# Performance work log

Measured on AMD Instinct MI355X. Metric: run time of the kernel, lower is better.

The kernel has to match this reference:

```python
import jax, jax.numpy as jnp
import numpy as np

U, DP, TOPK, NH = 2, 16, 8, 2
D = 512
M = DP ** U          # 256 slots
DK = U * DP          # 32 addressing dim
BETA_MAX = 2.0


def setup_inputs():
    key = jax.random.key(0)
    ks = jax.random.split(key, 12)
    B, T = 8, 128
    s = 0.02
    return {
        "h": jax.random.normal(ks[0], (B, T, D), jnp.float32),
        "K_slots": jax.random.normal(ks[1], (B, M, D), jnp.float32) * s,
        "V_slots": jax.random.normal(ks[2], (B, M, D), jnp.float32) * s,
        "z_K": jnp.ones((B, M), jnp.float32),
        "z_V": jnp.ones((B, M), jnp.float32),
        "W_k": jax.random.normal(ks[3], (DK, D), jnp.float32) * s,
        "W_q": jax.random.normal(ks[4], (DK, D), jnp.float32) * s,
        "log_tau_w": jnp.zeros((1,), jnp.float32),
        "log_tau_r": jnp.zeros((1,), jnp.float32),
        "hh_k": jax.random.normal(ks[5], (NH, D, D), jnp.float32) * s,
        "hh_vk": jax.random.normal(ks[6], (NH, D, D), jnp.float32) * s,
        "hh_vv": jax.random.normal(ks[7], (NH, D, D), jnp.float32) * s,
        "hh_bw": jax.random.normal(ks[8], (NH, 1, D), jnp.float32) * s,
        "hh_bb": jnp.zeros((NH, 1), jnp.float32),
        "gamma": jnp.float32(1.0),
        "W_out": jax.random.normal(ks[9], (D, D), jnp.float32) * s,
        "W_gate": jax.random.normal(ks[10], (D, D), jnp.float32) * s,
    }


def _kron_address(z, log_tau):
    # z: [B, DK]; Kronecker-factored softmax address over M = DP**U slots
    B = z.shape[0]
    probs = jax.nn.softmax(z.reshape(B, U, DP) / jnp.exp(log_tau[0]), axis=-1)
    addr = probs[:, 0]
    for u in range(1, U):
        addr = (addr[:, :, None] * probs[:, u, None, :]).reshape(B, -1)
    w, idx = jax.lax.top_k(addr, TOPK)
    return idx, w


def _forward(h, K_slots, V_slots, z_K, z_V, W_k, W_q, log_tau_w, log_tau_r,
             hh_k, hh_vk, hh_vv, hh_bw, hh_bb, gamma, W_out, W_gate,
             checkpoint=False):
    B, T, _ = h.shape
    scale = D ** -0.5
    b_idx = jnp.arange(B)[:, None]
    sp_gamma = jax.nn.softplus(gamma)

    def step(carry, h_t):
        K_s, V_s, zK, zV = carry
        write_idx, write_w = _kron_address(h_t @ W_k.T, log_tau_w)
        read_idx, _ = _kron_address(h_t @ W_q.T, log_tau_r)
        # scatter write weights into dense [B, M] (top-k indices are unique)
        w_full = jnp.zeros((B, M), h_t.dtype).at[b_idx, write_idx].set(write_w)
        # PDMA decay
        decay = (1.0 - w_full) ** sp_gamma
        K_s = decay[..., None] * K_s
        V_s = decay[..., None] * V_s
        zK = decay * zK + w_full
        zV = decay * zV + w_full
        # gather active slots: [B, K, D]
        K_act = jnp.take_along_axis(K_s, write_idx[:, :, None], axis=1)
        V_act = jnp.take_along_axis(V_s, write_idx[:, :, None], axis=1)
        # Householder update chain
        for j in range(NH):
            k_j = jax.nn.silu(h_t @ hh_k[j].T)
            k_hat = k_j / jnp.maximum(
                jnp.linalg.norm(k_j, axis=-1, keepdims=True), 1e-12)
            v_kj = h_t @ hh_vk[j].T
            v_vj = h_t @ hh_vv[j].T
            beta = BETA_MAX * jax.nn.sigmoid(h_t @ hh_bw[j].T + hh_bb[j])  # [B,1]
            kh = k_hat[:, None, :]
            be = beta[:, None, :]
            K_act = K_act - be * kh * (kh * K_act).sum(-1, keepdims=True) \
                    + be * k_j[:, None, :] * v_kj[:, None, :]
            V_act = V_act - be * kh * (kh * V_act).sum(-1, keepdims=True) \
                    + be * k_j[:, None, :] * v_vj[:, None, :]
        # scatter updated slots back
        K_s = K_s.at[b_idx, write_idx].set(K_act)
        V_s = V_s.at[b_idx, write_idx].set(V_act)
        # read path
        K_read = jnp.take_along_axis(K_s, read_idx[:, :, None], axis=1)
        V_read = jnp.take_along_axis(V_s, read_idx[:, :, None], axis=1)
        zK_read = jnp.take_along_axis(zK, read_idx, axis=1)[..., None]
        zV_read = jnp.take_along_axis(zV, read_idx, axis=1)[..., None]
        K_n = K_read / zK_read
        V_n = V_read / zV_read
        rel = (K_n * h_t[:, None, :]).sum(-1)           # [B, K]
        attn = jax.nn.softmax(rel * scale, axis=-1)
        readout = (attn[..., None] * V_n).sum(1)        # [B, D]
        out = jax.nn.sigmoid(h_t @ W_gate.T) * (readout @ W_out.T)
        return (K_s, V_s, zK, zV), (out, write_idx, read_idx)

    step_fn = jax.checkpoint(step) if checkpoint else step
    (K_s, V_s, zK, zV), (outs, widx, ridx) = jax.lax.scan(
        step_fn, (K_slots, V_slots, z_K, z_V), jnp.swapaxes(h, 0, 1))
    return (jnp.swapaxes(outs, 0, 1), K_s, V_s, zK, zV, widx[-1], ridx[-1])


def reference(h, K_slots, V_slots, z_K, z_V, W_k, W_q, log_tau_w, log_tau_r,
              hh_k, hh_vk, hh_vv, hh_bw, hh_bb, gamma, W_out, W_gate):
    return _forward(h, K_slots, V_slots, z_K, z_V, W_k, W_q, log_tau_w,
                    log_tau_r, hh_k, hh_vk, hh_vv, hh_bw, hh_bb, gamma,
                    W_out, W_gate)
```

## Files before the change

### kernel.cpp

```cpp
#include <hip/hip_runtime.h>
#include <math.h>

#define D_ 512
#define M_ 256
#define T_ 128
#define B_ 8
#define TOPK_ 8
#define NH_ 2
#define BT_ (B_*T_)

__device__ __forceinline__ float wred(float v){
#pragma unroll
  for (int m = 1; m < 64; m <<= 1) v += __shfl_xor(v, m, 64);
  return v;
}
__device__ __forceinline__ float4 ld4(const float* p){ return *(const float4*)p; }
__device__ __forceinline__ void st4(float* p, float4 v){ *(float4*)p = v; }
__device__ __forceinline__ float dot4(float4 a, float4 b){
  return a.x*b.x + a.y*b.y + a.z*b.z + a.w*b.w;
}
__device__ __forceinline__ float4 scl4(float4 a, float s){
  a.x*=s; a.y*=s; a.z*=s; a.w*=s; return a;
}
__device__ __forceinline__ float4 upd4(float4 r, float4 u0, float4 u1,
                                       float4 k0, float4 k1,
                                       float b0, float b1, float p0, float p1){
  r.x += b0*u0.x + b1*u1.x - p0*k0.x - p1*k1.x;
  r.y += b0*u0.y + b1*u1.y - p0*k0.y - p1*k1.y;
  r.z += b0*u0.z + b1*u1.z - p0*k0.z - p1*k1.z;
  r.w += b0*u0.w + b1*u1.w - p0*k0.w - p1*k1.w;
  return r;
}

__global__ __launch_bounds__(64) void addr_kernel(
    const float* __restrict__ h, const float* __restrict__ Wk,
    const float* __restrict__ Wq, const float* __restrict__ ltw,
    const float* __restrict__ ltr, const float* __restrict__ gammap,
    int* __restrict__ widxb, float* __restrict__ wwb,
    float* __restrict__ decb, int* __restrict__ ridxb)
{
  const int bt = blockIdx.x;
  const int tid = threadIdx.x;
  __shared__ float p_s[64];

  const float* hrow = h + (size_t)bt*D_;
  const float* wrow = (tid < 32) ? (Wk + (size_t)tid*D_)
                                 : (Wq + (size_t)(tid-32)*D_);
  float dot = 0.f;
  for (int d = 0; d < D_; d += 4){
    float4 hv = ld4(&hrow[d]); float4 wv = ld4(&wrow[d]);
    dot += hv.x*wv.x + hv.y*wv.y + hv.z*wv.z + hv.w*wv.w;
  }
  float tau = (tid < 32) ? expf(ltw[0]) : expf(ltr[0]);
  float mx = dot;
#pragma unroll
  for (int m = 1; m < 16; m <<= 1) mx = fmaxf(mx, __shfl_xor(mx, m, 64));
  float e = expf((dot - mx)/tau);
  float sm = e;
#pragma unroll
  for (int m = 1; m < 16; m <<= 1) sm += __shfl_xor(sm, m, 64);
  p_s[tid] = e / sm;
  __syncthreads();

  const int half = tid >> 5;
  const int l = tid & 31;
  const int g0 = half*32, g1 = half*32 + 16;
  float av[8];
#pragma unroll
  for (int k = 0; k < 8; ++k){
    int x = l*8 + k;
    av[k] = p_s[g0 + (x>>4)] * p_s[g1 + (x&15)];
  }
  const float sp = log1pf(expf(gammap[0]));
  for (int r = 0; r < TOPK_; ++r){
    float bv = -1.f; int bi = 0;
#pragma unroll
    for (int k = 0; k < 8; ++k){ if (av[k] > bv){ bv = av[k]; bi = l*8+k; } }
#pragma unroll
    for (int m = 1; m < 32; m <<= 1){
      float ov = __shfl_xor(bv, m, 64); int oi = __shfl_xor(bi, m, 64);
      if (ov > bv || (ov == bv && oi < bi)){ bv = ov; bi = oi; }
    }
    if ((bi >> 3) == l) av[bi & 7] = -2.f;
    if (tid == 0){
      widxb[bt*TOPK_+r] = bi; wwb[bt*TOPK_+r] = bv;
      decb[bt*TOPK_+r] = powf(1.f - bv, sp);
    }
    if (tid == 32) ridxb[bt*TOPK_+r] = bi;
  }
}

struct GemmPtrs { const float* W[6]; float* C[6]; };

__global__ __launch_bounds__(256) void gemm_nt(
    const float* __restrict__ A, GemmPtrs p)
{
  const float* W = p.W[blockIdx.z];
  float* C = p.C[blockIdx.z];
  const int n0 = blockIdx.x * 64;
  const int m0 = blockIdx.y * 64;
  const int tid = threadIdx.x;
  __shared__ __align__(16) float As[16][68];
  __shared__ __align__(16) float Bs[16][68];
  const int r  = tid >> 2;
  const int c4 = (tid & 3) << 2;
  const int tx4 = (tid & 15) << 2;
  const int ty4 = (tid >> 4) << 2;
  float acc[4][4] = {{0.f}};

  for (int kc = 0; kc < 512; kc += 16){
    float4 av = ld4(&A[(size_t)(m0+r)*512 + kc + c4]);
    float4 wv = ld4(&W[(size_t)(n0+r)*512 + kc + c4]);
    __syncthreads();
    As[c4+0][r]=av.x; As[c4+1][r]=av.y; As[c4+2][r]=av.z; As[c4+3][r]=av.w;
    Bs[c4+0][r]=wv.x; Bs[c4+1][r]=wv.y; Bs[c4+2][r]=wv.z; Bs[c4+3][r]=wv.w;
    __syncthreads();
#pragma unroll
    for (int k = 0; k < 16; ++k){
      float4 a  = ld4(&As[k][ty4]);
      float4 bq = ld4(&Bs[k][tx4]);
      acc[0][0]+=a.x*bq.x; acc[0][1]+=a.x*bq.y; acc[0][2]+=a.x*bq.z; acc[0][3]+=a.x*bq.w;
      acc[1][0]+=a.y*bq.x; acc[1][1]+=a.y*bq.y; acc[1][2]+=a.y*bq.z; acc[1][3]+=a.y*bq.w;
      acc[2][0]+=a.z*bq.x; acc[2][1]+=a.z*bq.y; acc[2][2]+=a.z*bq.z; acc[2][3]+=a.z*bq.w;
      acc[3][0]+=a.w*bq.x; acc[3][1]+=a.w*bq.y; acc[3][2]+=a.w*bq.z; acc[3][3]+=a.w*bq.w;
    }
  }
#pragma unroll
  for (int i = 0; i < 4; ++i){
    float4 cv; cv.x=acc[i][0]; cv.y=acc[i][1]; cv.z=acc[i][2]; cv.w=acc[i][3];
    st4(&C[(size_t)(m0+ty4+i)*512 + n0 + tx4], cv);
  }
}

__global__ __launch_bounds__(256) void gemm_out(
    const float* __restrict__ h, const float* __restrict__ rdo,
    const float* __restrict__ Wg, const float* __restrict__ Wo,
    float* __restrict__ C)
{
  const int n0 = blockIdx.x * 64;
  const int m0 = blockIdx.y * 64;
  const int tid = threadIdx.x;
  __shared__ __align__(16) float Ag[16][68];
  __shared__ __align__(16) float Ao[16][68];
  __shared__ __align__(16) float Bg[16][68];
  __shared__ __align__(16) float Bo[16][68];
  const int r  = tid >> 2;
  const int c4 = (tid & 3) << 2;
  const int tx4 = (tid & 15) << 2;
  const int ty4 = (tid >> 4) << 2;
  float accg[4][4] = {{0.f}};
  float acco[4][4] = {{0.f}};

  for (int kc = 0; kc < 512; kc += 16){
    float4 a1 = ld4(&h  [(size_t)(m0+r)*512 + kc + c4]);
    float4 a2 = ld4(&rdo[(size_t)(m0+r)*512 + kc + c4]);
    float4 w1 = ld4(&Wg [(size_t)(n0+r)*512 + kc + c4]);
    float4 w2 = ld4(&Wo [(size_t)(n0+r)*512 + kc + c4]);
    __syncthreads();
    Ag[c4+0][r]=a1.x; Ag[c4+1][r]=a1.y; Ag[c4+2][r]=a1.z; Ag[c4+3][r]=a1.w;
    Ao[c4+0][r]=a2.x; Ao[c4+1][r]=a2.y; Ao[c4+2][r]=a2.z; Ao[c4+3][r]=a2.w;
    Bg[c4+0][r]=w1.x; Bg[c4+1][r]=w1.y; Bg[c4+2][r]=w1.z; Bg[c4+3][r]=w1.w;
    Bo[c4+0][r]=w2.x; Bo[c4+1][r]=w2.y; Bo[c4+2][r]=w2.z; Bo[c4+3][r]=w2.w;
    __syncthreads();
#pragma unroll
    for (int k = 0; k < 16; ++k){
      float4 ag = ld4(&Ag[k][ty4]);
      float4 ao = ld4(&Ao[k][ty4]);
      float4 bg = ld4(&Bg[k][tx4]);
      float4 bo = ld4(&Bo[k][tx4]);
      accg[0][0]+=ag.x*bg.x; accg[0][1]+=ag.x*bg.y; accg[0][2]+=ag.x*bg.z; accg[0][3]+=ag.x*bg.w;
      accg[1][0]+=ag.y*bg.x; accg[1][1]+=ag.y*bg.y; accg[1][2]+=ag.y*bg.z; accg[1][3]+=ag.y*bg.w;
      accg[2][0]+=ag.z*bg.x; accg[2][1]+=ag.z*bg.y; accg[2][2]+=ag.z*bg.z; accg[2][3]+=ag.z*bg.w;
      accg[3][0]+=ag.w*bg.x; accg[3][1]+=ag.w*bg.y; accg[3][2]+=ag.w*bg.z; accg[3][3]+=ag.w*bg.w;
      acco[0][0]+=ao.x*bo.x; acco[0][1]+=ao.x*bo.y; acco[0][2]+=ao.x*bo.z; acco[0][3]+=ao.x*bo.w;
      acco[1][0]+=ao.y*bo.x; acco[1][1]+=ao.y*bo.y; acco[1][2]+=ao.y*bo.z; acco[1][3]+=ao.y*bo.w;
      acco[2][0]+=ao.z*bo.x; acco[2][1]+=ao.z*bo.y; acco[2][2]+=ao.z*bo.z; acco[2][3]+=ao.z*bo.w;
      acco[3][0]+=ao.w*bo.x; acco[3][1]+=ao.w*bo.y; acco[3][2]+=ao.w*bo.z; acco[3][3]+=ao.w*bo.w;
    }
  }
#pragma unroll
  for (int i = 0; i < 4; ++i){
    float4 cv;
    cv.x = acco[i][0] / (1.f + expf(-accg[i][0]));
    cv.y = acco[i][1] / (1.f + expf(-accg[i][1]));
    cv.z = acco[i][2] / (1.f + expf(-accg[i][2]));
    cv.w = acco[i][3] / (1.f + expf(-accg[i][3]));
    st4(&C[(size_t)(m0+ty4+i)*512 + n0 + tx4], cv);
  }
}

__global__ __launch_bounds__(256) void ew_kernel(
    float* __restrict__ khat, float* __restrict__ kvk, float* __restrict__ kvv,
    float* __restrict__ betab, const float* __restrict__ h,
    const float* __restrict__ hh_bw, const float* __restrict__ hh_bb)
{
  const int blk = blockIdx.x;
  const int j  = blk >> 10;
  const int bt = blk & 1023;
  const int tid = threadIdx.x;
  float* kp  = khat + (size_t)j*BT_*D_ + (size_t)bt*D_;
  float* vkp = kvk  + (size_t)j*BT_*D_ + (size_t)bt*D_;
  float* vvp = kvv  + (size_t)j*BT_*D_ + (size_t)bt*D_;
  const float* hp  = h + (size_t)bt*D_;
  const float* bwp = hh_bw + (size_t)j*D_;

  float s[2]; float nrm = 0.f, bd = 0.f;
#pragma unroll
  for (int q = 0; q < 2; ++q){
    int d = tid + q*256;
    float x = kp[d];
    float sv = x / (1.f + expf(-x));
    s[q] = sv; nrm += sv*sv; bd += hp[d]*bwp[d];
  }
  nrm = wred(nrm); bd = wred(bd);
  __shared__ float rb[8];
  int wid = tid >> 6, lane = tid & 63;
  if (lane == 0){ rb[wid] = nrm; rb[4+wid] = bd; }
  __syncthreads();
  float ns = rb[0]+rb[1]+rb[2]+rb[3];
  float bs = rb[4]+rb[5]+rb[6]+rb[7];
  float inv = 1.f / fmaxf(sqrtf(ns), 1e-12f);
#pragma unroll
  for (int q = 0; q < 2; ++q){
    int d = tid + q*256;
    float sv = s[q];
    kp[d]  = sv * inv;
    vkp[d] = sv * vkp[d];
    vvp[d] = sv * vvp[d];
  }
  if (tid == 0) betab[(size_t)j*BT_ + bt] = 2.f / (1.f + expf(-(bs + hh_bb[j])));
}

__global__ __launch_bounds__(64) void pre_kernel(
    const float* __restrict__ khat, const float* __restrict__ kvk,
    const float* __restrict__ kvv, float* __restrict__ preb)
{
  const int bt = blockIdx.x;
  const int lane = threadIdx.x;
  const float* k0 = khat + (size_t)bt*D_;
  const float* k1 = khat + (size_t)BT_*D_ + (size_t)bt*D_;
  const float* u0 = kvk + (size_t)bt*D_;
  const float* v0 = kvv + (size_t)bt*D_;
  float c = 0.f, dk = 0.f, dv = 0.f;
#pragma unroll
  for (int q = 0; q < 8; ++q){
    int d = lane*8 + q;
    float kv = k1[d];
    c += kv*k0[d]; dk += kv*u0[d]; dv += kv*v0[d];
  }
  c = wred(c); dk = wred(dk); dv = wred(dv);
  if (lane == 0){ preb[bt*4] = c; preb[bt*4+1] = dk; preb[bt*4+2] = dv; }
}

__global__ __launch_bounds__(512, 2) void scan_kernel(
    float* __restrict__ Ks, float* __restrict__ Vs,
    const float* __restrict__ zK0, const float* __restrict__ zV0,
    const float* __restrict__ khat, const float* __restrict__ kvkb,
    const float* __restrict__ kvvb, const float* __restrict__ betab,
    const float* __restrict__ preb,
    const int* __restrict__ widxb, const float* __restrict__ wwb,
    const float* __restrict__ decb, const int* __restrict__ ridxb,
    const float* __restrict__ h, float* __restrict__ readout,
    float* __restrict__ o_zK, float* __restrict__ o_zV,
    float* __restrict__ o_widx, float* __restrict__ o_ridx)
{
  __shared__ __align__(16) float ring[3][7*D_];
  __shared__ __align__(16) float fwdK[TOPK_][D_];
  __shared__ __align__(16) float fwdV[TOPK_][D_];
  __shared__ __align__(16) float Vr_s[TOPK_][D_];
  __shared__ float zK_s[M_], zV_s[M_];
  __shared__ float rel_s[TOPK_], zvr_s[TOPK_];

  const int b = blockIdx.x;
  const int tid = threadIdx.x;
  const int s = tid >> 6, lane = tid & 63;
  const int l4 = lane * 4;
  const float scale = 0.044194173824159216f;

  float* Ksb = Ks + (size_t)b*M_*D_;
  float* Vsb = Vs + (size_t)b*M_*D_;
  const float* vb[7] = { khat, khat + (size_t)BT_*D_,
                         kvkb, kvkb + (size_t)BT_*D_,
                         kvvb, kvvb + (size_t)BT_*D_, h };

  const int c0 = s, c1 = s + 8;
  const bool has1 = (c1 < 14);
  const float* src0 = vb[c0 >> 1];
  const float* src1 = vb[has1 ? (c1 >> 1) : 0];
  const int goff0 = (c0 & 1)*256 + l4;
  const int goff1 = (c1 & 1)*256 + l4;
  const int loff0 = (c0 >> 1)*D_ + goff0;
  const int loff1 = has1 ? ((c1 >> 1)*D_ + goff1) : 0;

  const int bt0 = b*T_;
  for (int tt = 0; tt < 2; ++tt){
    float4 a = ld4(src0 + (size_t)(bt0+tt)*D_ + goff0);
    st4(&ring[tt][loff0], a);
    if (has1){
      float4 c = ld4(src1 + (size_t)(bt0+tt)*D_ + goff1);
      st4(&ring[tt][loff1], c);
    }
  }
  float4 g0 = ld4(src0 + (size_t)(bt0+2)*D_ + goff0);
  float4 g1 = has1 ? ld4(src1 + (size_t)(bt0+2)*D_ + goff1)
                   : make_float4(0.f,0.f,0.f,0.f);

  int   mi  = widxb[bt0*TOPK_ + s];
  float ww  = wwb [bt0*TOPK_ + s];
  float dec = decb[bt0*TOPK_ + s];
  int   ri  = ridxb[bt0*TOPK_ + s];
  int   wv8 = widxb[bt0*TOPK_ + (lane & 7)];
  float be0 = betab[bt0], be1 = betab[BT_ + bt0];
  float c01 = preb[bt0*4], dKp = preb[bt0*4+1], dVp = preb[bt0*4+2];

  const int bt1 = bt0 + 1;
  int   mi_n  = widxb[bt1*TOPK_ + s];
  float ww_n  = wwb [bt1*TOPK_ + s];
  float dec_n = decb[bt1*TOPK_ + s];
  int   ri_n  = ridxb[bt1*TOPK_ + s];
  int   wv8_n = widxb[bt1*TOPK_ + (lane & 7)];
  float be0_n = betab[bt1], be1_n = betab[BT_ + bt1];
  float c01_n = preb[bt1*4], dKp_n = preb[bt1*4+1], dVp_n = preb[bt1*4+2];

  float4 K0 = ld4(&Ksb[(size_t)mi*D_ + l4]);
  float4 K1 = ld4(&Ksb[(size_t)mi*D_ + 256 + l4]);
  float4 V0 = ld4(&Vsb[(size_t)mi*D_ + l4]);
  float4 V1 = ld4(&Vsb[(size_t)mi*D_ + 256 + l4]);
  float4 RK0 = ld4(&Ksb[(size_t)ri*D_ + l4]);
  float4 RK1 = ld4(&Ksb[(size_t)ri*D_ + 256 + l4]);
  float4 RV0 = ld4(&Vsb[(size_t)ri*D_ + l4]);
  float4 RV1 = ld4(&Vsb[(size_t)ri*D_ + 256 + l4]);

  if (tid < M_){ zK_s[tid] = zK0[b*M_+tid]; zV_s[tid] = zV0[b*M_+tid]; }
  __syncthreads();

#pragma unroll 2
  for (int t = 0; t < T_; ++t){
    const int bt = b*T_ + t;
    const float* rbuf = ring[t % 3];

    float4 sKH0a = ld4(&rbuf[l4]),        sKH0b = ld4(&rbuf[256+l4]);
    float4 sKH1a = ld4(&rbuf[D_+l4]),     sKH1b = ld4(&rbuf[D_+256+l4]);
    float4 sUK0a = ld4(&rbuf[2*D_+l4]),   sUK0b = ld4(&rbuf[2*D_+256+l4]);
    float4 sUK1a = ld4(&rbuf[3*D_+l4]),   sUK1b = ld4(&rbuf[3*D_+256+l4]);
    float4 sUV0a = ld4(&rbuf[4*D_+l4]),   sUV0b = ld4(&rbuf[4*D_+256+l4]);
    float4 sUV1a = ld4(&rbuf[5*D_+l4]),   sUV1b = ld4(&rbuf[5*D_+256+l4]);
    float4 sHTa  = ld4(&rbuf[6*D_+l4]),   sHTb  = ld4(&rbuf[6*D_+256+l4]);

    if (t > 0){
      float rl[TOPK_];
#pragma unroll
      for (int i = 0; i < TOPK_; ++i) rl[i] = rel_s[i];
      float mx = rl[0];
#pragma unroll
      for (int i = 1; i < TOPK_; ++i) mx = fmaxf(mx, rl[i]);
      float smm = 0.f, r = 0.f;
#pragma unroll
      for (int i = 0; i < TOPK_; ++i){
        float ev = __expf(rl[i]-mx); smm += ev;
        r += ev * zvr_s[i] * Vr_s[i][tid];
      }
      readout[(size_t)(bt-1)*D_ + tid] = r / smm;
    }

    K0 = scl4(K0,dec); K1 = scl4(K1,dec);
    V0 = scl4(V0,dec); V1 = scl4(V1,dec);
    float aK = dot4(K0,sKH0a) + dot4(K1,sKH0b);
    float bK = dot4(K0,sKH1a) + dot4(K1,sKH1b);
    float aV = dot4(V0,sKH0a) + dot4(V1,sKH0b);
    float bV = dot4(V0,sKH1a) + dot4(V1,sKH1b);
#pragma unroll
    for (int m = 1; m < 64; m <<= 1){
      aK += __shfl_xor(aK,m,64); bK += __shfl_xor(bK,m,64);
      aV += __shfl_xor(aV,m,64); bV += __shfl_xor(bV,m,64);
    }
    float s1K = bK + be0*(dKp - aK*c01);
    float s1V = bV + be0*(dVp - aV*c01);
    float p0K = be0*aK, p1K = be1*s1K;
    float p0V = be0*aV, p1V = be1*s1V;
    K0 = upd4(K0, sUK0a, sUK1a, sKH0a, sKH1a, be0, be1, p0K, p1K);
    K1 = upd4(K1, sUK0b, sUK1b, sKH0b, sKH1b, be0, be1, p0K, p1K);
    V0 = upd4(V0, sUV0a, sUV1a, sKH0a, sKH1a, be0, be1, p0V, p1V);
    V1 = upd4(V1, sUV0b, sUV1b, sKH0b, sKH1b, be0, be1, p0V, p1V);

    st4(&fwdK[s][l4], K0); st4(&fwdK[s][256+l4], K1);
    st4(&fwdV[s][l4], V0); st4(&fwdV[s][256+l4], V1);
    st4(&Ksb[(size_t)mi*D_ + l4], K0); st4(&Ksb[(size_t)mi*D_ + 256 + l4], K1);
    st4(&Vsb[(size_t)mi*D_ + l4], V0); st4(&Vsb[(size_t)mi*D_ + 256 + l4], V1);
    if (lane == 0)      zK_s[mi] = dec*zK_s[mi] + ww;
    else if (lane == 1) zV_s[mi] = dec*zV_s[mi] + ww;
    __syncthreads();

    float* wbuf = ring[(t+2) % 3];
    st4(&wbuf[loff0], g0);
    if (has1) st4(&wbuf[loff1], g1);
    const int bt3 = (t+3 < T_) ? bt+3 : b*T_+T_-1;
    g0 = ld4(src0 + (size_t)bt3*D_ + goff0);
    if (has1) g1 = ld4(src1 + (size_t)bt3*D_ + goff1);

    float4 nK0 = ld4(&Ksb[(size_t)mi_n*D_ + l4]);
    float4 nK1 = ld4(&Ksb[(size_t)mi_n*D_ + 256 + l4]);
    float4 nV0 = ld4(&Vsb[(size_t)mi_n*D_ + l4]);
    float4 nV1 = ld4(&Vsb[(size_t)mi_n*D_ + 256 + l4]);
    float4 nRK0 = ld4(&Ksb[(size_t)ri_n*D_ + l4]);
    float4 nRK1 = ld4(&Ksb[(size_t)ri_n*D_ + 256 + l4]);
    float4 nRV0 = ld4(&Vsb[(size_t)ri_n*D_ + l4]);
    float4 nRV1 = ld4(&Vsb[(size_t)ri_n*D_ + 256 + l4]);

    const int btnn = (t+2 < T_) ? bt+2 : b*T_+T_-1;
    int   mi_nn  = widxb[btnn*TOPK_ + s];
    float ww_nn  = wwb [btnn*TOPK_ + s];
    float dec_nn = decb[btnn*TOPK_ + s];
    int   ri_nn  = ridxb[btnn*TOPK_ + s];
    int   wv8_nn = widxb[btnn*TOPK_ + (lane & 7)];
    float be0_nn = betab[btnn], be1_nn = betab[BT_ + btnn];
    float c01_nn = preb[btnn*4], dKp_nn = preb[btnn*4+1], dVp_nn = preb[btnn*4+2];

    unsigned long long mk = __ballot((lane < 8) && (wv8 == ri));
    float4 rk0, rk1, rv0, rv1;
    if (mk){
      int fm = __ffsll(mk) - 1;
      rk0 = ld4(&fwdK[fm][l4]); rk1 = ld4(&fwdK[fm][256+l4]);
      rv0 = ld4(&fwdV[fm][l4]); rv1 = ld4(&fwdV[fm][256+l4]);
    } else {
      rk0 = RK0; rk1 = RK1; rv0 = RV0; rv1 = RV1;
    }
    float dt = dot4(rk0,sHTa) + dot4(rk1,sHTb);
    dt = wred(dt);
    st4(&Vr_s[s][l4], rv0); st4(&Vr_s[s][256+l4], rv1);
    if (lane == 0){
      rel_s[s] = dt * scale / zK_s[ri];
      zvr_s[s] = 1.0f / zV_s[ri];
    }

    __builtin_amdgcn_s_waitcnt(0xc07f);
    __builtin_amdgcn_s_barrier();

    K0=nK0; K1=nK1; V0=nV0; V1=nV1;
    RK0=nRK0; RK1=nRK1; RV0=nRV0; RV1=nRV1;
    mi=mi_n; ww=ww_n; dec=dec_n; ri=ri_n; wv8=wv8_n;
    be0=be0_n; be1=be1_n; c01=c01_n; dKp=dKp_n; dVp=dVp_n;
    mi_n=mi_nn; ww_n=ww_nn; dec_n=dec_nn; ri_n=ri_nn; wv8_n=wv8_nn;
    be0_n=be0_nn; be1_n=be1_nn; c01_n=c01_nn; dKp_n=dKp_nn; dVp_n=dVp_nn;
  }

  {
    const int btL = b*T_ + T_ - 1;
    float rl[TOPK_];
#pragma unroll
    for (int i = 0; i < TOPK_; ++i) rl[i] = rel_s[i];
    float mx = rl[0];
#pragma unroll
    for (int i = 1; i < TOPK_; ++i) mx = fmaxf(mx, rl[i]);
    float smm = 0.f, r = 0.f;
#pragma unroll
    for (int i = 0; i < TOPK_; ++i){
      float ev = __expf(rl[i]-mx); smm += ev;
      r += ev * zvr_s[i] * Vr_s[i][tid];
    }
    readout[(size_t)btL*D_ + tid] = r / smm;

    if (tid < M_){ o_zK[b*M_+tid] = zK_s[tid]; o_zV[b*M_+tid] = zV_s[tid]; }
    if (tid < TOPK_){
      o_widx[b*TOPK_+tid] = (float)widxb[btL*TOPK_ + tid];
      o_ridx[b*TOPK_+tid] = (float)ridxb[btL*TOPK_ + tid];
    }
  }
}

extern "C" void kernel_launch(void* const* d_in, const int* in_sizes, int n_in,
                              void* d_out, int out_size, void* d_ws, size_t ws_size,
                              hipStream_t stream)
{
  (void)in_sizes; (void)n_in; (void)out_size; (void)ws_size;
  const float* h       = (const float*)d_in[0];
  const float* K_slots = (const float*)d_in[1];
  const float* V_slots = (const float*)d_in[2];
  const float* z_K     = (const float*)d_in[3];
  const float* z_V     = (const float*)d_in[4];
  const float* W_k     = (const float*)d_in[5];
  const float* W_q     = (const float*)d_in[6];
  const float* ltw     = (const float*)d_in[7];
  const float* ltr     = (const float*)d_in[8];
  const float* hh_k    = (const float*)d_in[9];
  const float* hh_vk   = (const float*)d_in[10];
  const float* hh_vv   = (const float*)d_in[11];
  const float* hh_bw   = (const float*)d_in[12];
  const float* hh_bb   = (const float*)d_in[13];
  const float* gamma   = (const float*)d_in[14];
  const float* W_out   = (const float*)d_in[15];
  const float* W_gate  = (const float*)d_in[16];

  float* out    = (float*)d_out;
  float* o_outs = out;
  float* o_Ks   = out + 524288;
  float* o_Vs   = out + 1572864;
  float* o_zK   = out + 2621440;
  float* o_zV   = out + 2623488;
  float* o_widx = out + 2625536;
  float* o_ridx = out + 2625600;

  float* ws    = (float*)d_ws;
  float* khat  = ws;
  float* kvk   = ws + 2*(size_t)BT_*D_;
  float* kvv   = kvk + 2*(size_t)BT_*D_;
  float* rdo   = kvv + 2*(size_t)BT_*D_;
  float* betab = rdo + (size_t)BT_*D_;
  float* wwb   = betab + 2*BT_;
  float* decb  = wwb + BT_*TOPK_;
  int*   widxb = (int*)(decb + BT_*TOPK_);
  int*   ridxb = widxb + BT_*TOPK_;
  float* preb  = (float*)(ridxb + BT_*TOPK_);

  hipMemcpyAsync(o_Ks, K_slots, sizeof(float)*(size_t)B_*M_*D_,
                 hipMemcpyDeviceToDevice, stream);
  hipMemcpyAsync(o_Vs, V_slots, sizeof(float)*(size_t)B_*M_*D_,
                 hipMemcpyDeviceToDevice, stream);

  addr_kernel<<<BT_, 64, 0, stream>>>(h, W_k, W_q, ltw, ltr, gamma,
                                      widxb, wwb, decb, ridxb);

  GemmPtrs p{};
  p.W[0] = hh_k;           p.C[0] = khat;
  p.W[1] = hh_k + 262144;  p.C[1] = khat + (size_t)BT_*D_;
  p.W[2] = hh_vk;          p.C[2] = kvk;
  p.W[3] = hh_vk + 262144; p.C[3] = kvk + (size_t)BT_*D_;
  p.W[4] = hh_vv;          p.C[4] = kvv;
  p.W[5] = hh_vv + 262144; p.C[5] = kvv + (size_t)BT_*D_;
  gemm_nt<<<dim3(8,16,6), 256, 0, stream>>>(h, p);

  ew_kernel<<<2*BT_, 256, 0, stream>>>(khat, kvk, kvv, betab, h, hh_bw, hh_bb);
  pre_kernel<<<BT_, 64, 0, stream>>>(khat, kvk, kvv, preb);

  scan_kernel<<<B_, 512, 0, stream>>>(o_Ks, o_Vs, z_K, z_V, khat, kvk, kvv,
                                      betab, preb, widxb, wwb, decb, ridxb,
                                      h, rdo, o_zK, o_zV, o_widx, o_ridx);

  gemm_out<<<dim3(8,16), 256, 0, stream>>>(h, rdo, W_gate, W_out, o_outs);
}
```

Baseline: 576.2 us.

## Fuse elementwise and pre-dot kernels, shrink scan ring, add DPP reductions

Merges ew_kernel and pre_kernel into one per-row kernel that also folds the beta-weighted combination of both heads' value updates into a single precomputed vector. The scan's LDS ring therefore drops from 7 to 4 vectors per step, with h read directly from global. Per-step metadata is packed into float4 records, and wave reductions use DPP adds plus readlane instead of shuffles. The scan also writes forwarded rows only when a later read or write needs them and takes the next slot from LDS when it is found there. The cost of all this is more complex control flow in the serial scan and possible rounding differences from the changed reduction order.

New measurement: 510.5 us. 11.4% less time.

```diff
diff --git a/kernel.cpp b/kernel.cpp
--- a/kernel.cpp
+++ b/kernel.cpp
@@ -22,22 +22,31 @@
 __device__ __forceinline__ float4 scl4(float4 a, float s){
   a.x*=s; a.y*=s; a.z*=s; a.w*=s; return a;
 }
-__device__ __forceinline__ float4 upd4(float4 r, float4 u0, float4 u1,
-                                       float4 k0, float4 k1,
-                                       float b0, float b1, float p0, float p1){
-  r.x += b0*u0.x + b1*u1.x - p0*k0.x - p1*k1.x;
-  r.y += b0*u0.y + b1*u1.y - p0*k0.y - p1*k1.y;
-  r.z += b0*u0.z + b1*u1.z - p0*k0.z - p1*k1.z;
-  r.w += b0*u0.w + b1*u1.w - p0*k0.w - p1*k1.w;
-  return r;
+
+template<int CTRL>
+__device__ __forceinline__ float dpp_add(float x){
+  int y = __builtin_amdgcn_update_dpp(0, __float_as_int(x), CTRL, 0xf, 0xf, true);
+  return x + __int_as_float(y);
+}
+__device__ __forceinline__ float wredd(float x){
+  x = dpp_add<0x111>(x);
+  x = dpp_add<0x112>(x);
+  x = dpp_add<0x114>(x);
+  x = dpp_add<0x118>(x);
+  x = dpp_add<0x142>(x);
+  x = dpp_add<0x143>(x);
+  return __int_as_float(__builtin_amdgcn_readlane(__float_as_int(x), 63));
+}
+
+__device__ __forceinline__ void bar_lgkm(){
+  asm volatile("s_waitcnt lgkmcnt(0)\n\ts_barrier" ::: "memory");
 }
 
 __global__ __launch_bounds__(64) void addr_kernel(
     const float* __restrict__ h, const float* __restrict__ Wk,
     const float* __restrict__ Wq, const float* __restrict__ ltw,
     const float* __restrict__ ltr, const float* __restrict__ gammap,
-    int* __restrict__ widxb, float* __restrict__ wwb,
-    float* __restrict__ decb, int* __restrict__ ridxb)
+    float* __restrict__ metab)
 {
   const int bt = blockIdx.x;
   const int tid = threadIdx.x;
@@ -82,11 +91,11 @@
       if (ov > bv || (ov == bv && oi < bi)){ bv = ov; bi = oi; }
     }
     if ((bi >> 3) == l) av[bi & 7] = -2.f;
+    float* mp = metab + (size_t)(bt*TOPK_ + r)*4;
     if (tid == 0){
-      widxb[bt*TOPK_+r] = bi; wwb[bt*TOPK_+r] = bv;
-      decb[bt*TOPK_+r] = powf(1.f - bv, sp);
-    }
-    if (tid == 32) ridxb[bt*TOPK_+r] = bi;
+      mp[0] = __int_as_float(bi); mp[1] = bv; mp[2] = powf(1.f - bv, sp);
+    }
+    if (tid == 32) mp[3] = __int_as_float(bi);
   }
 }
 
@@ -189,87 +198,88 @@
   }
 }
 
-__global__ __launch_bounds__(256) void ew_kernel(
+__global__ __launch_bounds__(256) void ew2_kernel(
     float* __restrict__ khat, float* __restrict__ kvk, float* __restrict__ kvv,
-    float* __restrict__ betab, const float* __restrict__ h,
+    float* __restrict__ pre2, const float* __restrict__ h,
     const float* __restrict__ hh_bw, const float* __restrict__ hh_bb)
 {
-  const int blk = blockIdx.x;
-  const int j  = blk >> 10;
-  const int bt = blk & 1023;
+  const int bt = blockIdx.x;
   const int tid = threadIdx.x;
-  float* kp  = khat + (size_t)j*BT_*D_ + (size_t)bt*D_;
-  float* vkp = kvk  + (size_t)j*BT_*D_ + (size_t)bt*D_;
-  float* vvp = kvv  + (size_t)j*BT_*D_ + (size_t)bt*D_;
+  const int wid = tid >> 6, lane = tid & 63;
+  float* k0p  = khat + (size_t)bt*D_;
+  float* k1p  = khat + (size_t)BT_*D_ + (size_t)bt*D_;
+  float* vk0p = kvk  + (size_t)bt*D_;
+  float* vk1p = kvk  + (size_t)BT_*D_ + (size_t)bt*D_;
+  float* vv0p = kvv  + (size_t)bt*D_;
+  float* vv1p = kvv  + (size_t)BT_*D_ + (size_t)bt*D_;
   const float* hp  = h + (size_t)bt*D_;
-  const float* bwp = hh_bw + (size_t)j*D_;
-
-  float s[2]; float nrm = 0.f, bd = 0.f;
+
+  float s0[2], s1[2];
+  float n0 = 0.f, n1 = 0.f, bd0 = 0.f, bd1 = 0.f;
 #pragma unroll
   for (int q = 0; q < 2; ++q){
     int d = tid + q*256;
-    float x = kp[d];
-    float sv = x / (1.f + expf(-x));
-    s[q] = sv; nrm += sv*sv; bd += hp[d]*bwp[d];
-  }
-  nrm = wred(nrm); bd = wred(bd);
-  __shared__ float rb[8];
-  int wid = tid >> 6, lane = tid & 63;
-  if (lane == 0){ rb[wid] = nrm; rb[4+wid] = bd; }
+    float x0 = k0p[d], x1 = k1p[d], hv = hp[d];
+    float v0 = x0 / (1.f + expf(-x0));
+    float v1 = x1 / (1.f + expf(-x1));
+    s0[q] = v0; s1[q] = v1;
+    n0 += v0*v0; n1 += v1*v1;
+    bd0 += hv*hh_bw[d]; bd1 += hv*hh_bw[D_ + d];
+  }
+  __shared__ float4 rb[4];
+  float4 acc = make_float4(wred(n0), wred(n1), wred(bd0), wred(bd1));
+  if (lane == 0) rb[wid] = acc;
   __syncthreads();
-  float ns = rb[0]+rb[1]+rb[2]+rb[3];
-  float bs = rb[4]+rb[5]+rb[6]+rb[7];
-  float inv = 1.f / fmaxf(sqrtf(ns), 1e-12f);
+  float4 t0 = rb[0], t1 = rb[1], t2 = rb[2], t3 = rb[3];
+  n0 = t0.x+t1.x+t2.x+t3.x; n1 = t0.y+t1.y+t2.y+t3.y;
+  bd0 = t0.z+t1.z+t2.z+t3.z; bd1 = t0.w+t1.w+t2.w+t3.w;
+  float inv0 = 1.f / fmaxf(sqrtf(n0), 1e-12f);
+  float inv1 = 1.f / fmaxf(sqrtf(n1), 1e-12f);
+  float be0 = 2.f / (1.f + expf(-(bd0 + hh_bb[0])));
+  float be1 = 2.f / (1.f + expf(-(bd1 + hh_bb[1])));
+
+  float c01 = 0.f, dK = 0.f, dV = 0.f;
 #pragma unroll
   for (int q = 0; q < 2; ++q){
     int d = tid + q*256;
-    float sv = s[q];
-    kp[d]  = sv * inv;
-    vkp[d] = sv * vkp[d];
-    vvp[d] = sv * vvp[d];
-  }
-  if (tid == 0) betab[(size_t)j*BT_ + bt] = 2.f / (1.f + expf(-(bs + hh_bb[j])));
-}
-
-__global__ __launch_bounds__(64) void pre_kernel(
-    const float* __restrict__ khat, const float* __restrict__ kvk,
-    const float* __restrict__ kvv, float* __restrict__ preb)
-{
-  const int bt = blockIdx.x;
-  const int lane = threadIdx.x;
-  const float* k0 = khat + (size_t)bt*D_;
-  const float* k1 = khat + (size_t)BT_*D_ + (size_t)bt*D_;
-  const float* u0 = kvk + (size_t)bt*D_;
-  const float* v0 = kvv + (size_t)bt*D_;
-  float c = 0.f, dk = 0.f, dv = 0.f;
-#pragma unroll
-  for (int q = 0; q < 8; ++q){
-    int d = lane*8 + q;
-    float kv = k1[d];
-    c += kv*k0[d]; dk += kv*u0[d]; dv += kv*v0[d];
-  }
-  c = wred(c); dk = wred(dk); dv = wred(dv);
-  if (lane == 0){ preb[bt*4] = c; preb[bt*4+1] = dk; preb[bt*4+2] = dv; }
+    float kh0 = s0[q]*inv0, kh1 = s1[q]*inv1;
+    float u0K = s0[q]*vk0p[d], u1K = s1[q]*vk1p[d];
+    float u0V = s0[q]*vv0p[d], u1V = s1[q]*vv1p[d];
+    k0p[d] = kh0; k1p[d] = kh1;
+    vk0p[d] = be0*u0K + be1*u1K;
+    vv0p[d] = be0*u0V + be1*u1V;
+    c01 += kh1*kh0; dK += kh1*u0K; dV += kh1*u0V;
+  }
+  __syncthreads();
+  float4 acc2 = make_float4(wred(c01), wred(dK), wred(dV), 0.f);
+  if (lane == 0) rb[wid] = acc2;
+  __syncthreads();
+  if (tid == 0){
+    float4 a = rb[0], b = rb[1], c = rb[2], d = rb[3];
+    pre2[(size_t)bt*8+0] = a.x+b.x+c.x+d.x;
+    pre2[(size_t)bt*8+1] = a.y+b.y+c.y+d.y;
+    pre2[(size_t)bt*8+2] = a.z+b.z+c.z+d.z;
+    pre2[(size_t)bt*8+3] = be0;
+    pre2[(size_t)bt*8+4] = be1;
+  }
 }
 
 __global__ __launch_bounds__(512, 2) void scan_kernel(
     float* __restrict__ Ks, float* __restrict__ Vs,
     const float* __restrict__ zK0, const float* __restrict__ zV0,
-    const float* __restrict__ khat, const float* __restrict__ kvkb,
-    const float* __restrict__ kvvb, const float* __restrict__ betab,
-    const float* __restrict__ preb,
-    const int* __restrict__ widxb, const float* __restrict__ wwb,
-    const float* __restrict__ decb, const int* __restrict__ ridxb,
-    const float* __restrict__ h, float* __restrict__ readout,
+    const float* __restrict__ khat, const float* __restrict__ ucKb,
+    const float* __restrict__ ucVb, const float* __restrict__ pre2,
+    const float* __restrict__ metab, const float* __restrict__ h,
+    float* __restrict__ readout,
     float* __restrict__ o_zK, float* __restrict__ o_zV,
     float* __restrict__ o_widx, float* __restrict__ o_ridx)
 {
-  __shared__ __align__(16) float ring[3][7*D_];
+  __shared__ __align__(16) float ring[3][4*D_];
   __shared__ __align__(16) float fwdK[TOPK_][D_];
   __shared__ __align__(16) float fwdV[TOPK_][D_];
   __shared__ __align__(16) float Vr_s[TOPK_][D_];
   __shared__ float zK_s[M_], zV_s[M_];
-  __shared__ float rel_s[TOPK_], zvr_s[TOPK_];
+  __shared__ float2 rel2_s[TOPK_];
 
   const int b = blockIdx.x;
   const int tid = threadIdx.x;
@@ -279,48 +289,34 @@
 
   float* Ksb = Ks + (size_t)b*M_*D_;
   float* Vsb = Vs + (size_t)b*M_*D_;
-  const float* vb[7] = { khat, khat + (size_t)BT_*D_,
-                         kvkb, kvkb + (size_t)BT_*D_,
-                         kvvb, kvvb + (size_t)BT_*D_, h };
-
-  const int c0 = s, c1 = s + 8;
-  const bool has1 = (c1 < 14);
-  const float* src0 = vb[c0 >> 1];
-  const float* src1 = vb[has1 ? (c1 >> 1) : 0];
-  const int goff0 = (c0 & 1)*256 + l4;
-  const int goff1 = (c1 & 1)*256 + l4;
-  const int loff0 = (c0 >> 1)*D_ + goff0;
-  const int loff1 = has1 ? ((c1 >> 1)*D_ + goff1) : 0;
+  const float* vbt[4] = { khat, khat + (size_t)BT_*D_, ucKb, ucVb };
+  const float* srcc = vbt[s >> 1];
+  const int goff = (s & 1)*256 + l4;
+  const int loff = (s >> 1)*D_ + goff;
+  const float4* mb = (const float4*)metab;
 
   const int bt0 = b*T_;
-  for (int tt = 0; tt < 2; ++tt){
-    float4 a = ld4(src0 + (size_t)(bt0+tt)*D_ + goff0);
-    st4(&ring[tt][loff0], a);
-    if (has1){
-      float4 c = ld4(src1 + (size_t)(bt0+tt)*D_ + goff1);
-      st4(&ring[tt][loff1], c);
-    }
-  }
-  float4 g0 = ld4(src0 + (size_t)(bt0+2)*D_ + goff0);
-  float4 g1 = has1 ? ld4(src1 + (size_t)(bt0+2)*D_ + goff1)
-                   : make_float4(0.f,0.f,0.f,0.f);
-
-  int   mi  = widxb[bt0*TOPK_ + s];
-  float ww  = wwb [bt0*TOPK_ + s];
-  float dec = decb[bt0*TOPK_ + s];
-  int   ri  = ridxb[bt0*TOPK_ + s];
-  int   wv8 = widxb[bt0*TOPK_ + (lane & 7)];
-  float be0 = betab[bt0], be1 = betab[BT_ + bt0];
-  float c01 = preb[bt0*4], dKp = preb[bt0*4+1], dVp = preb[bt0*4+2];
+  for (int tt = 0; tt < 2; ++tt)
+    st4(&ring[tt][loff], ld4(srcc + (size_t)(bt0+tt)*D_ + goff));
+  float4 g = ld4(srcc + (size_t)(bt0+2)*D_ + goff);
+
+  float4 me   = mb[bt0*TOPK_ + s];
+  float4 me8  = mb[bt0*TOPK_ + (lane & 7)];
+  int   mi  = __float_as_int(me.x);  float ww  = me.y;  float dec = me.z;
+  int   ri  = __float_as_int(me.w);
+  int   wv8 = __float_as_int(me8.x); int rv8 = __float_as_int(me8.w);
+  float4 pm = *(const float4*)&pre2[(size_t)bt0*8];
+  float be1v = pre2[(size_t)bt0*8+4];
+  float c01 = pm.x, dKp = pm.y, dVp = pm.z, be0 = pm.w;
 
   const int bt1 = bt0 + 1;
-  int   mi_n  = widxb[bt1*TOPK_ + s];
-  float ww_n  = wwb [bt1*TOPK_ + s];
-  float dec_n = decb[bt1*TOPK_ + s];
-  int   ri_n  = ridxb[bt1*TOPK_ + s];
-  int   wv8_n = widxb[bt1*TOPK_ + (lane & 7)];
-  float be0_n = betab[bt1], be1_n = betab[BT_ + bt1];
-  float c01_n = preb[bt1*4], dKp_n = preb[bt1*4+1], dVp_n = preb[bt1*4+2];
+  float4 me_n  = mb[bt1*TOPK_ + s];
+  float4 me8_n = mb[bt1*TOPK_ + (lane & 7)];
+  int   mi_n  = __float_as_int(me_n.x);  float ww_n = me_n.y;
+  float dec_n = me_n.z;                  int ri_n  = __float_as_int(me_n.w);
+  int   wv8_n = __float_as_int(me8_n.x); int rv8_n = __float_as_int(me8_n.w);
+  float4 pm_n = *(const float4*)&pre2[(size_t)bt1*8];
+  float be1_n = pre2[(size_t)bt1*8+4];
 
   float4 K0 = ld4(&Ksb[(size_t)mi*D_ + l4]);
   float4 K1 = ld4(&Ksb[(size_t)mi*D_ + 256 + l4]);
@@ -334,87 +330,108 @@
   if (tid < M_){ zK_s[tid] = zK0[b*M_+tid]; zV_s[tid] = zV0[b*M_+tid]; }
   __syncthreads();
 
-#pragma unroll 2
   for (int t = 0; t < T_; ++t){
     const int bt = b*T_ + t;
     const float* rbuf = ring[t % 3];
 
-    float4 sKH0a = ld4(&rbuf[l4]),        sKH0b = ld4(&rbuf[256+l4]);
-    float4 sKH1a = ld4(&rbuf[D_+l4]),     sKH1b = ld4(&rbuf[D_+256+l4]);
-    float4 sUK0a = ld4(&rbuf[2*D_+l4]),   sUK0b = ld4(&rbuf[2*D_+256+l4]);
-    float4 sUK1a = ld4(&rbuf[3*D_+l4]),   sUK1b = ld4(&rbuf[3*D_+256+l4]);
-    float4 sUV0a = ld4(&rbuf[4*D_+l4]),   sUV0b = ld4(&rbuf[4*D_+256+l4]);
-    float4 sUV1a = ld4(&rbuf[5*D_+l4]),   sUV1b = ld4(&rbuf[5*D_+256+l4]);
-    float4 sHTa  = ld4(&rbuf[6*D_+l4]),   sHTb  = ld4(&rbuf[6*D_+256+l4]);
+    float4 HTa = ld4(h + (size_t)bt*D_ + l4);
+    float4 HTb = ld4(h + (size_t)bt*D_ + 256 + l4);
+
+    float4 kh0a = ld4(&rbuf[l4]),        kh0b = ld4(&rbuf[256+l4]);
+    float4 kh1a = ld4(&rbuf[D_+l4]),     kh1b = ld4(&rbuf[D_+256+l4]);
+    float4 ucKa = ld4(&rbuf[2*D_+l4]),   ucKb2 = ld4(&rbuf[2*D_+256+l4]);
+    float4 ucVa = ld4(&rbuf[3*D_+l4]),   ucVb2 = ld4(&rbuf[3*D_+256+l4]);
 
     if (t > 0){
-      float rl[TOPK_];
-#pragma unroll
-      for (int i = 0; i < TOPK_; ++i) rl[i] = rel_s[i];
-      float mx = rl[0];
-#pragma unroll
-      for (int i = 1; i < TOPK_; ++i) mx = fmaxf(mx, rl[i]);
+      float2 rz[TOPK_];
+#pragma unroll
+      for (int i = 0; i < TOPK_; ++i) rz[i] = rel2_s[i];
+      float mx = rz[0].x;
+#pragma unroll
+      for (int i = 1; i < TOPK_; ++i) mx = fmaxf(mx, rz[i].x);
       float smm = 0.f, r = 0.f;
 #pragma unroll
       for (int i = 0; i < TOPK_; ++i){
-        float ev = __expf(rl[i]-mx); smm += ev;
-        r += ev * zvr_s[i] * Vr_s[i][tid];
+        float ev = __expf(rz[i].x - mx); smm += ev;
+        r += ev * rz[i].y * Vr_s[i][tid];
       }
       readout[(size_t)(bt-1)*D_ + tid] = r / smm;
     }
 
     K0 = scl4(K0,dec); K1 = scl4(K1,dec);
     V0 = scl4(V0,dec); V1 = scl4(V1,dec);
-    float aK = dot4(K0,sKH0a) + dot4(K1,sKH0b);
-    float bK = dot4(K0,sKH1a) + dot4(K1,sKH1b);
-    float aV = dot4(V0,sKH0a) + dot4(V1,sKH0b);
-    float bV = dot4(V0,sKH1a) + dot4(V1,sKH1b);
-#pragma unroll
-    for (int m = 1; m < 64; m <<= 1){
-      aK += __shfl_xor(aK,m,64); bK += __shfl_xor(bK,m,64);
-      aV += __shfl_xor(aV,m,64); bV += __shfl_xor(bV,m,64);
-    }
-    float s1K = bK + be0*(dKp - aK*c01);
-    float s1V = bV + be0*(dVp - aV*c01);
-    float p0K = be0*aK, p1K = be1*s1K;
-    float p0V = be0*aV, p1V = be1*s1V;
-    K0 = upd4(K0, sUK0a, sUK1a, sKH0a, sKH1a, be0, be1, p0K, p1K);
-    K1 = upd4(K1, sUK0b, sUK1b, sKH0b, sKH1b, be0, be1, p0K, p1K);
-    V0 = upd4(V0, sUV0a, sUV1a, sKH0a, sKH1a, be0, be1, p0V, p1V);
-    V1 = upd4(V1, sUV0b, sUV1b, sKH0b, sKH1b, be0, be1, p0V, p1V);
-
-    st4(&fwdK[s][l4], K0); st4(&fwdK[s][256+l4], K1);
-    st4(&fwdV[s][l4], V0); st4(&fwdV[s][256+l4], V1);
+    float aK = wredd(dot4(K0,kh0a) + dot4(K1,kh0b));
+    float bK = wredd(dot4(K0,kh1a) + dot4(K1,kh1b));
+    float aV = wredd(dot4(V0,kh0a) + dot4(V1,kh0b));
+    float bV = wredd(dot4(V0,kh1a) + dot4(V1,kh1b));
+    float p0K = be0*aK, p1K = be1v*(bK + be0*(dKp - aK*c01));
+    float p0V = be0*aV, p1V = be1v*(bV + be0*(dVp - aV*c01));
+    K0.x += ucKa.x  - p0K*kh0a.x - p1K*kh1a.x;
+    K0.y += ucKa.y  - p0K*kh0a.y - p1K*kh1a.y;
+    K0.z += ucKa.z  - p0K*kh0a.z - p1K*kh1a.z;
+    K0.w += ucKa.w  - p0K*kh0a.w - p1K*kh1a.w;
+    K1.x += ucKb2.x - p0K*kh0b.x - p1K*kh1b.x;
+    K1.y += ucKb2.y - p0K*kh0b.y - p1K*kh1b.y;
+    K1.z += ucKb2.z - p0K*kh0b.z - p1K*kh1b.z;
+    K1.w += ucKb2.w - p0K*kh0b.w - p1K*kh1b.w;
+    V0.x += ucVa.x  - p0V*kh0a.x - p1V*kh1a.x;
+    V0.y += ucVa.y  - p0V*kh0a.y - p1V*kh1a.y;
+    V0.z += ucVa.z  - p0V*kh0a.z - p1V*kh1a.z;
+    V0.w += ucVa.w  - p0V*kh0a.w - p1V*kh1a.w;
+    V1.x += ucVb2.x - p0V*kh0b.x - p1V*kh1b.x;
+    V1.y += ucVb2.y - p0V*kh0b.y - p1V*kh1b.y;
+    V1.z += ucVb2.z - p0V*kh0b.z - p1V*kh1b.z;
+    V1.w += ucVb2.w - p0V*kh0b.w - p1V*kh1b.w;
+
+    unsigned long long nf =
+        __ballot((lane < 8) && (rv8   == mi)) |
+        __ballot((lane < 8) && (wv8_n == mi)) |
+        __ballot((lane < 8) && (rv8_n == mi));
+    if (nf){
+      st4(&fwdK[s][l4], K0); st4(&fwdK[s][256+l4], K1);
+      st4(&fwdV[s][l4], V0); st4(&fwdV[s][256+l4], V1);
+    }
     st4(&Ksb[(size_t)mi*D_ + l4], K0); st4(&Ksb[(size_t)mi*D_ + 256 + l4], K1);
     st4(&Vsb[(size_t)mi*D_ + l4], V0); st4(&Vsb[(size_t)mi*D_ + 256 + l4], V1);
     if (lane == 0)      zK_s[mi] = dec*zK_s[mi] + ww;
     else if (lane == 1) zV_s[mi] = dec*zV_s[mi] + ww;
-    __syncthreads();
-
-    float* wbuf = ring[(t+2) % 3];
-    st4(&wbuf[loff0], g0);
-    if (has1) st4(&wbuf[loff1], g1);
+
+    bar_lgkm();
+
+    st4(&ring[(t+2)%3][loff], g);
     const int bt3 = (t+3 < T_) ? bt+3 : b*T_+T_-1;
-    g0 = ld4(src0 + (size_t)bt3*D_ + goff0);
-    if (has1) g1 = ld4(src1 + (size_t)bt3*D_ + goff1);
-
-    float4 nK0 = ld4(&Ksb[(size_t)mi_n*D_ + l4]);
-    float4 nK1 = ld4(&Ksb[(size_t)mi_n*D_ + 256 + l4]);
-    float4 nV0 = ld4(&Vsb[(size_t)mi_n*D_ + l4]);
-    float4 nV1 = ld4(&Vsb[(size_t)mi_n*D_ + 256 + l4]);
-    float4 nRK0 = ld4(&Ksb[(size_t)ri_n*D_ + l4]);
-    float4 nRK1 = ld4(&Ksb[(size_t)ri_n*D_ + 256 + l4]);
-    float4 nRV0 = ld4(&Vsb[(size_t)ri_n*D_ + l4]);
-    float4 nRV1 = ld4(&Vsb[(size_t)ri_n*D_ + 256 + l4]);
+    g = ld4(srcc + (size_t)bt3*D_ + goff);
+
+    unsigned long long hS = __ballot((lane < 8) && (wv8 == mi_n));
+    float4 nK0, nK1, nV0, nV1;
+    if (hS){
+      int w = __ffsll(hS) - 1;
+      nK0 = ld4(&fwdK[w][l4]); nK1 = ld4(&fwdK[w][256+l4]);
+      nV0 = ld4(&fwdV[w][l4]); nV1 = ld4(&fwdV[w][256+l4]);
+    } else {
+      nK0 = ld4(&Ksb[(size_t)mi_n*D_ + l4]);
+      nK1 = ld4(&Ksb[(size_t)mi_n*D_ + 256 + l4]);
+      nV0 = ld4(&Vsb[(size_t)mi_n*D_ + l4]);
+      nV1 = ld4(&Vsb[(size_t)mi_n*D_ + 256 + l4]);
+    }
+    unsigned long long hR = __ballot((lane < 8) && (wv8 == ri_n));
+    float4 nRK0, nRK1, nRV0, nRV1;
+    if (hR){
+      int w = __ffsll(hR) - 1;
+      nRK0 = ld4(&fwdK[w][l4]); nRK1 = ld4(&fwdK[w][256+l4]);
+      nRV0 = ld4(&fwdV[w][l4]); nRV1 = ld4(&fwdV[w][256+l4]);
+    } else {
+      nRK0 = ld4(&Ksb[(size_t)ri_n*D_ + l4]);
+      nRK1 = ld4(&Ksb[(size_t)ri_n*D_ + 256 + l4]);
+      nRV0 = ld4(&Vsb[(size_t)ri_n*D_ + l4]);
+      nRV1 = ld4(&Vsb[(size_t)ri_n*D_ + 256 + l4]);
+    }
 
     const int btnn = (t+2 < T_) ? bt+2 : b*T_+T_-1;
-    int   mi_nn  = widxb[btnn*TOPK_ + s];
-    float ww_nn  = wwb [btnn*TOPK_ + s];
-    float dec_nn = decb[btnn*TOPK_ + s];
-    int   ri_nn  = ridxb[btnn*TOPK_ + s];
-    int   wv8_nn = widxb[btnn*TOPK_ + (lane & 7)];
-    float be0_nn = betab[btnn], be1_nn = betab[BT_ + btnn];
-    float c01_nn = preb[btnn*4], dKp_nn = preb[btnn*4+1], dVp_nn = preb[btnn*4+2];
+    float4 me_nn  = mb[btnn*TOPK_ + s];
+    float4 me8_nn = mb[btnn*TOPK_ + (lane & 7)];
+    float4 pm_nn  = *(const float4*)&pre2[(size_t)btnn*8];
+    float  be1_nn = pre2[(size_t)btnn*8+4];
 
     unsigned long long mk = __ballot((lane < 8) && (wv8 == ri));
     float4 rk0, rk1, rv0, rv1;
@@ -425,45 +442,44 @@
     } else {
       rk0 = RK0; rk1 = RK1; rv0 = RV0; rv1 = RV1;
     }
-    float dt = dot4(rk0,sHTa) + dot4(rk1,sHTb);
-    dt = wred(dt);
+    float dt = wredd(dot4(rk0,HTa) + dot4(rk1,HTb));
     st4(&Vr_s[s][l4], rv0); st4(&Vr_s[s][256+l4], rv1);
-    if (lane == 0){
-      rel_s[s] = dt * scale / zK_s[ri];
-      zvr_s[s] = 1.0f / zV_s[ri];
-    }
-
-    __builtin_amdgcn_s_waitcnt(0xc07f);
-    __builtin_amdgcn_s_barrier();
+    if (lane == 0)
+      rel2_s[s] = make_float2(dt * scale / zK_s[ri], 1.0f / zV_s[ri]);
+
+    __syncthreads();
 
     K0=nK0; K1=nK1; V0=nV0; V1=nV1;
     RK0=nRK0; RK1=nRK1; RV0=nRV0; RV1=nRV1;
-    mi=mi_n; ww=ww_n; dec=dec_n; ri=ri_n; wv8=wv8_n;
-    be0=be0_n; be1=be1_n; c01=c01_n; dKp=dKp_n; dVp=dVp_n;
-    mi_n=mi_nn; ww_n=ww_nn; dec_n=dec_nn; ri_n=ri_nn; wv8_n=wv8_nn;
-    be0_n=be0_nn; be1_n=be1_nn; c01_n=c01_nn; dKp_n=dKp_nn; dVp_n=dVp_nn;
+    mi=mi_n; ww=ww_n; dec=dec_n; ri=ri_n; wv8=wv8_n; rv8=rv8_n;
+    c01=pm_n.x; dKp=pm_n.y; dVp=pm_n.z; be0=pm_n.w; be1v=be1_n;
+    mi_n=__float_as_int(me_nn.x); ww_n=me_nn.y; dec_n=me_nn.z;
+    ri_n=__float_as_int(me_nn.w);
+    wv8_n=__float_as_int(me8_nn.x); rv8_n=__float_as_int(me8_nn.w);
+    pm_n=pm_nn; be1_n=be1_nn;
   }
 
   {
     const int btL = b*T_ + T_ - 1;
-    float rl[TOPK_];
-#pragma unroll
-    for (int i = 0; i < TOPK_; ++i) rl[i] = rel_s[i];
-    float mx = rl[0];
-#pragma unroll
-    for (int i = 1; i < TOPK_; ++i) mx = fmaxf(mx, rl[i]);
+    float2 rz[TOPK_];
+#pragma unroll
+    for (int i = 0; i < TOPK_; ++i) rz[i] = rel2_s[i];
+    float mx = rz[0].x;
+#pragma unroll
+    for (int i = 1; i < TOPK_; ++i) mx = fmaxf(mx, rz[i].x);
     float smm = 0.f, r = 0.f;
 #pragma unroll
     for (int i = 0; i < TOPK_; ++i){
-      float ev = __expf(rl[i]-mx); smm += ev;
-      r += ev * zvr_s[i] * Vr_s[i][tid];
+      float ev = __expf(rz[i].x - mx); smm += ev;
+      r += ev * rz[i].y * Vr_s[i][tid];
     }
     readout[(size_t)btL*D_ + tid] = r / smm;
 
     if (tid < M_){ o_zK[b*M_+tid] = zK_s[tid]; o_zV[b*M_+tid] = zV_s[tid]; }
     if (tid < TOPK_){
-      o_widx[b*TOPK_+tid] = (float)widxb[btL*TOPK_ + tid];
-      o_ridx[b*TOPK_+tid] = (float)ridxb[btL*TOPK_ + tid];
+      float4 m = mb[btL*TOPK_ + tid];
+      o_widx[b*TOPK_+tid] = (float)__float_as_int(m.x);
+      o_ridx[b*TOPK_+tid] = (float)__float_as_int(m.w);
     }
   }
 }
@@ -505,20 +521,15 @@
   float* kvk   = ws + 2*(size_t)BT_*D_;
   float* kvv   = kvk + 2*(size_t)BT_*D_;
   float* rdo   = kvv + 2*(size_t)BT_*D_;
-  float* betab = rdo + (size_t)BT_*D_;
-  float* wwb   = betab + 2*BT_;
-  float* decb  = wwb + BT_*TOPK_;
-  int*   widxb = (int*)(decb + BT_*TOPK_);
-  int*   ridxb = widxb + BT_*TOPK_;
-  float* preb  = (float*)(ridxb + BT_*TOPK_);
-
-  hipMemcpyAsync(o_Ks, K_slots, sizeof(float)*(size_t)B_*M_*D_,
-                 hipMemcpyDeviceToDevice, stream);
-  hipMemcpyAsync(o_Vs, V_slots, sizeof(float)*(size_t)B_*M_*D_,
-                 hipMemcpyDeviceToDevice, stream);
-
-  addr_kernel<<<BT_, 64, 0, stream>>>(h, W_k, W_q, ltw, ltr, gamma,
-                                      widxb, wwb, decb, ridxb);
+  float* metab = rdo + (size_t)BT_*D_;
+  float* pre2  = metab + (size_t)BT_*TOPK_*4;
+
+  (void)hipMemcpyAsync(o_Ks, K_slots, sizeof(float)*(size_t)B_*M_*D_,
+                       hipMemcpyDeviceToDevice, stream);
+  (void)hipMemcpyAsync(o_Vs, V_slots, sizeof(float)*(size_t)B_*M_*D_,
+                       hipMemcpyDeviceToDevice, stream);
+
+  addr_kernel<<<BT_, 64, 0, stream>>>(h, W_k, W_q, ltw, ltr, gamma, metab);
 
   GemmPtrs p{};
   p.W[0] = hh_k;           p.C[0] = khat;
@@ -529,12 +540,11 @@
   p.W[5] = hh_vv + 262144; p.C[5] = kvv + (size_t)BT_*D_;
   gemm_nt<<<dim3(8,16,6), 256, 0, stream>>>(h, p);
 
-  ew_kernel<<<2*BT_, 256, 0, stream>>>(khat, kvk, kvv, betab, h, hh_bw, hh_bb);
-  pre_kernel<<<BT_, 64, 0, stream>>>(khat, kvk, kvv, preb);
+  ew2_kernel<<<BT_, 256, 0, stream>>>(khat, kvk, kvv, pre2, h, hh_bw, hh_bb);
 
   scan_kernel<<<B_, 512, 0, stream>>>(o_Ks, o_Vs, z_K, z_V, khat, kvk, kvv,
-                                      betab, preb, widxb, wwb, decb, ridxb,
-                                      h, rdo, o_zK, o_zV, o_widx, o_ridx);
+                                      pre2, metab, h, rdo,
+                                      o_zK, o_zV, o_widx, o_ridx);
 
   gemm_out<<<dim3(8,16), 256, 0, stream>>>(h, rdo, W_gate, W_out, o_outs);
 }
```
